# Performance work log

Hardware: AMD Instinct MI355X
Metric: run time of the kernel (lower is better)

## Reference

```python
import jax, jax.numpy as jnp
import numpy as np

N_HEAD = 12


def setup_inputs() -> dict:
    key = jax.random.key(0)
    k1, k2, k3 = jax.random.split(key, 3)
    B, T, C = 1, 4096, 768
    x = jax.random.normal(k1, (B, T, C), dtype=jnp.float32)
    w_attn = jax.random.normal(k2, (C, 3 * C), dtype=jnp.float32) * (1.0 / np.sqrt(C))
    w_proj = jax.random.normal(k3, (C, C), dtype=jnp.float32) * (1.0 / np.sqrt(C))
    return {"x": x, "w_attn": w_attn, "w_proj": w_proj}


def reference(x, w_attn, w_proj):
    B, T, C = x.shape
    hd = C // N_HEAD
    qkv = x @ w_attn  # [B, T, 3C]
    q, k, v = jnp.split(qkv, 3, axis=-1)
    # [B, H, T, hd]
    q = q.reshape(B, T, N_HEAD, hd).transpose(0, 2, 1, 3)
    k = k.reshape(B, T, N_HEAD, hd).transpose(0, 2, 1, 3)
    v = v.reshape(B, T, N_HEAD, hd).transpose(0, 2, 1, 3)
    scale = 1.0 / np.sqrt(hd).astype(np.float32)
    att = jnp.einsum('bhtd,bhsd->bhts', q, k) * scale  # materialized TxT scores
    causal = jnp.tril(jnp.ones((T, T), dtype=bool))
    att = jnp.where(causal[None, None], att, -jnp.inf)
    att = jax.nn.softmax(att, axis=-1)
    y = jnp.einsum('bhts,bhsd->bhtd', att, v)  # [B, H, T, hd]
    y = y.transpose(0, 2, 1, 3).reshape(B, T, C)
    return y @ w_proj
```

## Files before the change

kernel.cpp:

```cpp
#include <hip/hip_runtime.h>


typedef short bf16x8 __attribute__((ext_vector_type(8)));
typedef float f32x4 __attribute__((ext_vector_type(4)));

#define T_SEQ 4096
#define C_DIM 768
#define NH 12
#define HD 64

__device__ __forceinline__ unsigned short f2bf(float f) {
  union { float f; unsigned u; } v; v.f = f;
  unsigned r = v.u + 0x7FFFu + ((v.u >> 16) & 1u);
  return (unsigned short)(r >> 16);
}
__device__ __forceinline__ float bf2f(unsigned short u) {
  union { unsigned u; float f; } v; v.u = ((unsigned)u) << 16;
  return v.f;
}
__device__ __forceinline__ unsigned cvtpk(float a, float b) {
  unsigned r;
  asm("v_cvt_pk_bf16_f32 %0, %1, %2" : "=v"(r) : "v"(a), "v"(b));
  return r;
}
#define E2(x) __builtin_amdgcn_exp2f(x)

#define GLD16(g, l) __builtin_amdgcn_global_load_lds( \
    (const __attribute__((address_space(1))) void*)(g), \
    (__attribute__((address_space(3))) void*)(l), 16, 0, 0)

__device__ __forceinline__ void tr_body(const float* __restrict__ in,
                                        unsigned short* __restrict__ out,
                                        int R, int Cc, int bx, int by,
                                        float (*tile)[33]) {
  int tx = threadIdx.x & 31, ty = threadIdx.x >> 5;
#pragma unroll
  for (int i = 0; i < 32; i += 8)
    tile[ty + i][tx] = in[(size_t)(by * 32 + ty + i) * Cc + bx * 32 + tx];
  __syncthreads();
#pragma unroll
  for (int i = 0; i < 32; i += 8)
    out[(size_t)(bx * 32 + ty + i) * R + by * 32 + tx] = f2bf(tile[tx][ty + i]);
}

__global__ void prep(const float* __restrict__ x, unsigned short* __restrict__ Xb,
                     const float* __restrict__ w_attn, unsigned short* __restrict__ WaT,
                     const float* __restrict__ w_proj, unsigned short* __restrict__ WpT) {
  __shared__ float tile[32][33];
  const int bid = blockIdx.x;
  if (bid < 3072) {
    int i = (bid * 256 + threadIdx.x) * 4;
    float4 v = *reinterpret_cast<const float4*>(x + i);
    ushort4 o;
    o.x = f2bf(v.x); o.y = f2bf(v.y); o.z = f2bf(v.z); o.w = f2bf(v.w);
    *reinterpret_cast<ushort4*>(Xb + i) = o;
  } else if (bid < 3072 + 1728) {
    int b = bid - 3072;
    tr_body(w_attn, WaT, 768, 2304, b % 72, b / 72, tile);
  } else {
    int b = bid - 4800;
    tr_body(w_proj, WpT, 768, 768, b % 24, b / 24, tile);
  }
}

template <int MODE, int BM, int BN>
__global__ __launch_bounds__(256, 4)
void gemm_bt(const unsigned short* __restrict__ A,
             const unsigned short* __restrict__ Bt,
             void* __restrict__ out0,
             unsigned short* __restrict__ Kout,
             unsigned short* __restrict__ Vt,
             int M, int N, int K) {
  __shared__ __align__(16) unsigned short As[BM * 64];
  __shared__ __align__(16) unsigned short Bs[BN * 64];
  constexpr int AM = BM / 32, AN = BN / 32;
  const int nbn = N / BN;
  const int nwg = (M / BM) * nbn;
  const int cpx = nwg >> 3;
  const int swz = ((int)blockIdx.x & 7) * cpx + ((int)blockIdx.x >> 3);
  const int bm = swz / nbn, bn = swz % nbn;
  const int tid = threadIdx.x;
  const int wid = tid >> 6, lane = tid & 63;
  const int wr = wid >> 1, wc = wid & 1;
  const int lr = lane & 15;
  const int lk8 = (lane >> 4) * 8;
  const int rsub = lane >> 3, csub = (lane & 7) * 8;

  f32x4 acc[AM][AN] = {};

  const int nk = K / 64;
  for (int kt = 0; kt < nk; ++kt) {
    __syncthreads();
    {
      const unsigned short* gA = A + (size_t)(bm * BM) * K + kt * 64;
      const unsigned short* gB = Bt + (size_t)(bn * BN) * K + kt * 64;
#pragma unroll
      for (int c = 0; c < BM / 32; ++c) {
        int seg = wid * (BM / 32) + c;
        int row = seg * 8 + rsub;
        GLD16(gA + (size_t)row * K + csub, (char*)As + seg * 1024);
      }
#pragma unroll
      for (int c = 0; c < BN / 32; ++c) {
        int seg = wid * (BN / 32) + c;
        int row = seg * 8 + rsub;
        GLD16(gB + (size_t)row * K + csub, (char*)Bs + seg * 1024);
      }
    }
    __syncthreads();
#pragma unroll
    for (int kk = 0; kk < 2; ++kk) {
      bf16x8 a[AM], b[AN];
      int lk = kk * 32 + lk8;
#pragma unroll
      for (int m = 0; m < AM; ++m)
        a[m] = *reinterpret_cast<const bf16x8*>(&As[(wr * (BM / 2) + m * 16 + lr) * 64 + lk]);
#pragma unroll
      for (int n = 0; n < AN; ++n)
        b[n] = *reinterpret_cast<const bf16x8*>(&Bs[(wc * (BN / 2) + n * 16 + lr) * 64 + lk]);
#pragma unroll
      for (int m = 0; m < AM; ++m)
#pragma unroll
        for (int n = 0; n < AN; ++n)
          acc[m][n] = __builtin_amdgcn_mfma_f32_16x16x32_bf16(a[m], b[n], acc[m][n], 0, 0, 0);
    }
  }

  const int row0 = bm * BM + wr * (BM / 2);
  const int col0 = bn * BN + wc * (BN / 2);
  const int g = lane >> 4;

  if constexpr (MODE == 0) {
    if (bn * BN >= 1536) {
      __shared__ unsigned short Vst[64][72];
      const int dl0 = wc * (BN / 2);
      const int tl0 = wr * (BM / 2);
#pragma unroll
      for (int m = 0; m < AM; ++m)
#pragma unroll
        for (int n = 0; n < AN; ++n) {
          uint2 pk;
          pk.x = cvtpk(acc[m][n][0], acc[m][n][1]);
          pk.y = cvtpk(acc[m][n][2], acc[m][n][3]);
          *reinterpret_cast<uint2*>(&Vst[dl0 + n * 16 + lr][tl0 + m * 16 + g * 4]) = pk;
        }
      __syncthreads();
      const int dl = tid >> 2;
      const int tb = (tid & 3) * 16;
      uint4 a0 = *reinterpret_cast<const uint4*>(&Vst[dl][tb]);
      uint4 a1 = *reinterpret_cast<const uint4*>(&Vst[dl][tb + 8]);
      unsigned short* dst = Vt + (size_t)(bn * BN - 1536 + dl) * M + bm * BM + tb;
      *reinterpret_cast<uint4*>(dst) = a0;
      *reinterpret_cast<uint4*>(dst + 8) = a1;
      return;
    }
  }

#pragma unroll
  for (int m = 0; m < AM; ++m)
#pragma unroll
    for (int n = 0; n < AN; ++n)
#pragma unroll
      for (int j = 0; j < 4; ++j) {
        int r = row0 + m * 16 + g * 4 + j;
        int c = col0 + n * 16 + lr;
        float v = acc[m][n][j];
        if (MODE == 0) {
          if (c < 768)
            ((unsigned short*)out0)[(size_t)r * 768 + c] = f2bf(v * 0.180336884f);
          else
            Kout[(size_t)r * 768 + (c - 768)] = f2bf(v);
        } else {
          ((float*)out0)[(size_t)r * N + c] = v;
        }
      }
}

__device__ __forceinline__ void stage_k(const unsigned short* __restrict__ Kb,
                                        unsigned short* Kbuf,
                                        int h, int st, int wid, int lane) {
  const int cg = lane & 7, rsub = (lane >> 3) & 7;
  const unsigned short* gK = Kb + (size_t)(st * 64) * C_DIM + h * 64;
#pragma unroll
  for (int c = 0; c < 2; ++c) {
    int seg = wid * 2 + c;
    int row = seg * 8 + rsub;
    GLD16(gK + (size_t)row * C_DIM + (cg ^ rsub) * 8, (char*)Kbuf + seg * 1024);
  }
}
__device__ __forceinline__ void stage_v(const unsigned short* __restrict__ Vt,
                                        unsigned short* Vbuf,
                                        int h, int st, int wid, int lane) {
  const int cg = lane & 7, rsub = (lane >> 3) & 7;
  const unsigned short* gV = Vt + (size_t)(h * 64) * T_SEQ + st * 64;
#pragma unroll
  for (int c = 0; c < 2; ++c) {
    int seg = wid * 2 + c;
    int row = seg * 8 + rsub;
    GLD16(gV + (size_t)row * T_SEQ + (cg ^ rsub) * 8, (char*)Vbuf + seg * 1024);
  }
}

__device__ __forceinline__ int nchunks(int q) { return (2 * q + 13) / 12; }
__device__ __forceinline__ int part_off(int qb) {
  if (qb < 12) return (qb - 6) * 2;
  if (qb < 18) return 12 + (qb - 12) * 3;
  if (qb < 24) return 30 + (qb - 18) * 4;
  if (qb < 30) return 54 + (qb - 24) * 5;
  return 84 + (qb - 30) * 6;
}
__device__ __forceinline__ unsigned short* part_ptr(char* pA, char* pB, int set) {
  return (set < 768) ? (unsigned short*)(pA + (size_t)set * 16384)
                     : (unsigned short*)(pB + (size_t)(set - 768) * 16384);
}

__global__ __launch_bounds__(256, 3)
void attn_fwd(const unsigned short* __restrict__ Qb,
              const unsigned short* __restrict__ Kb,
              const unsigned short* __restrict__ Vt,
              unsigned short* __restrict__ Y,
              char* __restrict__ partA, char* __restrict__ partB,
              float* __restrict__ ml) {
  __shared__ __align__(16) unsigned short Ks[2][64 * 64];
  __shared__ __align__(16) unsigned short Vs[64 * 64];
  __shared__ __align__(16) unsigned short Ps[4][32 * 64];

  const int h = blockIdx.x;
  int qb = 0, ck = 0;
  {
    int idx = blockIdx.y;
    for (int q = 31; q >= 0; --q) {
      int nc = nchunks(q);
      if (idx < nc) { qb = q; ck = idx; break; }
      idx -= nc;
    }
  }
  const int nch = nchunks(qb);
  const int q0 = qb * 128;
  const int nst_total = 2 * qb + 2;
  const int st0 = ck * 12;
  const int st1 = (st0 + 12 < nst_total) ? st0 + 12 : nst_total;

  const int tid = threadIdx.x;
  const int wid = tid >> 6, lane = tid & 63;
  const int l15 = lane & 15, g = lane >> 4;
  const int sw = l15 & 7;
  const int qw = q0 + wid * 32;

  bf16x8 qf[2][2];
#pragma unroll
  for (int m = 0; m < 2; ++m)
#pragma unroll
    for (int kk = 0; kk < 2; ++kk)
      qf[m][kk] = *reinterpret_cast<const bf16x8*>(
          &Qb[(size_t)(qw + m * 16 + l15) * C_DIM + h * 64 + kk * 32 + g * 8]);

  bf16x8 ones;
#pragma unroll
  for (int e = 0; e < 8; ++e) ones[e] = (short)0x3F80;

  f32x4 o[2][4] = {};
  f32x4 po[2] = {};
  float mrow[2] = {-1e30f, -1e30f};

  stage_k(Kb, Ks[0], h, st0, wid, lane);
  stage_v(Vt, Vs, h, st0, wid, lane);
  int cur = 0;

  for (int st = st0; st < st1; ++st) {
    const bool haveNext = (st + 1 < st1);
    if (haveNext) {
      stage_k(Kb, Ks[cur ^ 1], h, st + 1, wid, lane);
      asm volatile("s_waitcnt vmcnt(2)" ::: "memory");
    } else {
      asm volatile("s_waitcnt vmcnt(0)" ::: "memory");
    }
    __builtin_amdgcn_s_barrier();

    const bool active = (st * 64) <= (qw + 31);
    if (active) {
      const unsigned short* K_ = Ks[cur];

      f32x4 sT[2][4] = {};
      __builtin_amdgcn_s_setprio(1);
#pragma unroll
      for (int kk = 0; kk < 2; ++kk) {
        bf16x8 kf[4];
#pragma unroll
        for (int n = 0; n < 4; ++n)
          kf[n] = *reinterpret_cast<const bf16x8*>(
              &K_[(n * 16 + l15) * 64 + (((kk * 4 + g) ^ sw) * 8)]);
#pragma unroll
        for (int m = 0; m < 2; ++m)
#pragma unroll
          for (int n = 0; n < 4; ++n)
            sT[m][n] = __builtin_amdgcn_mfma_f32_16x16x32_bf16(kf[n], qf[m][kk], sT[m][n], 0, 0, 0);
      }
      __builtin_amdgcn_s_setprio(0);

      unsigned short* Pw = Ps[wid];
#pragma unroll
      for (int m = 0; m < 2; ++m) {
        if (!(st * 64 + 63 <= qw + m * 16)) {
          const int bound = (qw + m * 16 + l15) - st * 64;
#pragma unroll
          for (int n = 0; n < 4; ++n)
#pragma unroll
            for (int jj = 0; jj < 4; ++jj) {
              int sl = n * 16 + g * 4 + jj;
              if (sl > bound) sT[m][n][jj] = -1e30f;
            }
        }
        float vm[4];
#pragma unroll
        for (int n = 0; n < 4; ++n)
          vm[n] = fmaxf(fmaxf(sT[m][n][0], sT[m][n][1]), fmaxf(sT[m][n][2], sT[m][n][3]));
        float vmax = fmaxf(fmaxf(vm[0], vm[1]), fmaxf(vm[2], vm[3]));
        vmax = fmaxf(vmax, __shfl_xor(vmax, 16, 64));
        vmax = fmaxf(vmax, __shfl_xor(vmax, 32, 64));
        const bool defer = (__all(vmax <= mrow[m] + 8.0f) != 0);
        const float mnew = defer ? mrow[m] : fmaxf(mrow[m], vmax);
#pragma unroll
        for (int n = 0; n < 4; ++n)
#pragma unroll
          for (int jj = 0; jj < 4; ++jj)
            sT[m][n][jj] = E2(sT[m][n][jj] - mnew);
        if (!defer) {
          float alpha = E2(mrow[m] - mnew);
          mrow[m] = mnew;
#pragma unroll
          for (int n2 = 0; n2 < 4; ++n2) o[m][n2] *= alpha;
          po[m] *= alpha;
        }
#pragma unroll
        for (int n = 0; n < 4; ++n) {
          uint2 pw;
          pw.x = cvtpk(sT[m][n][0], sT[m][n][1]);
          pw.y = cvtpk(sT[m][n][2], sT[m][n][3]);
          *reinterpret_cast<uint2*>(
              &Pw[(m * 16 + l15) * 64 + (((n * 2 + (g >> 1)) ^ sw) * 8) + (g & 1) * 4]) = pw;
        }
      }
      asm volatile("s_waitcnt lgkmcnt(0)" ::: "memory");

      __builtin_amdgcn_s_setprio(1);
#pragma unroll
      for (int ks = 0; ks < 2; ++ks) {
        bf16x8 vf[4], pf[2];
#pragma unroll
        for (int n2 = 0; n2 < 4; ++n2)
          vf[n2] = *reinterpret_cast<const bf16x8*>(
              &Vs[(n2 * 16 + l15) * 64 + (((ks * 4 + g) ^ sw) * 8)]);
#pragma unroll
        for (int m = 0; m < 2; ++m)
          pf[m] = *reinterpret_cast<const bf16x8*>(
              &Pw[(m * 16 + l15) * 64 + (((ks * 4 + g) ^ sw) * 8)]);
#pragma unroll
        for (int m = 0; m < 2; ++m) {
#pragma unroll
          for (int n2 = 0; n2 < 4; ++n2)
            o[m][n2] = __builtin_amdgcn_mfma_f32_16x16x32_bf16(vf[n2], pf[m], o[m][n2], 0, 0, 0);
          po[m] = __builtin_amdgcn_mfma_f32_16x16x32_bf16(ones, pf[m], po[m], 0, 0, 0);
        }
      }
      __builtin_amdgcn_s_setprio(0);
    }
    asm volatile("" ::: "memory");
    __builtin_amdgcn_s_barrier();
    if (haveNext) stage_v(Vt, Vs, h, st + 1, wid, lane);
    cur ^= 1;
  }

  if (nch == 1) {
#pragma unroll
    for (int m = 0; m < 2; ++m) {
      float inv = 1.0f / po[m][0];
      int qg = qw + m * 16 + l15;
#pragma unroll
      for (int n2 = 0; n2 < 4; ++n2) {
        uint2 yk;
        yk.x = cvtpk(o[m][n2][0] * inv, o[m][n2][1] * inv);
        yk.y = cvtpk(o[m][n2][2] * inv, o[m][n2][3] * inv);
        *reinterpret_cast<uint2*>(&Y[(size_t)qg * C_DIM + h * 64 + n2 * 16 + g * 4]) = yk;
      }
    }
  } else {
    const int set = h * 96 + part_off(qb) + ck;
    unsigned short* po_ = part_ptr(partA, partB, set);
#pragma unroll
    for (int m = 0; m < 2; ++m) {
      int qL = wid * 32 + m * 16 + l15;
#pragma unroll
      for (int n2 = 0; n2 < 4; ++n2) {
        uint2 pk;
        pk.x = cvtpk(o[m][n2][0], o[m][n2][1]);
        pk.y = cvtpk(o[m][n2][2], o[m][n2][3]);
        *reinterpret_cast<uint2*>(&po_[qL * 64 + n2 * 16 + g * 4]) = pk;
      }
      if (g == 0) {
        ml[(size_t)set * 256 + qL * 2] = mrow[m];
        ml[(size_t)set * 256 + qL * 2 + 1] = po[m][0];
      }
    }
  }
}

__global__ __launch_bounds__(256)
void attn_combine(char* __restrict__ partA, char* __restrict__ partB,
                  const float* __restrict__ ml, unsigned short* __restrict__ Y) {
  const int qb = 6 + blockIdx.x;
  const int h = blockIdx.y;
  const int nch = nchunks(qb);
  const int set0 = h * 96 + part_off(qb);
  const int t = threadIdx.x;
  const int r = t >> 1, dh = (t & 1) * 32;

  float mi[6], li[6];
  float M = -1e30f;
  for (int i = 0; i < nch; ++i) {
    mi[i] = ml[(size_t)(set0 + i) * 256 + r * 2];
    li[i] = ml[(size_t)(set0 + i) * 256 + r * 2 + 1];
    M = fmaxf(M, mi[i]);
  }
  float L = 0.f;
  float O[32];
#pragma unroll
  for (int d = 0; d < 32; ++d) O[d] = 0.f;
  for (int i = 0; i < nch; ++i) {
    float w = E2(mi[i] - M);
    L += li[i] * w;
    const unsigned short* po = part_ptr(partA, partB, set0 + i) + r * 64 + dh;
#pragma unroll
    for (int d4 = 0; d4 < 32; d4 += 4) {
      ushort4 v = *reinterpret_cast<const ushort4*>(po + d4);
      O[d4 + 0] += bf2f(v.x) * w;
      O[d4 + 1] += bf2f(v.y) * w;
      O[d4 + 2] += bf2f(v.z) * w;
      O[d4 + 3] += bf2f(v.w) * w;
    }
  }
  float inv = 1.0f / L;
  unsigned short* yp = Y + (size_t)(qb * 128 + r) * C_DIM + h * 64 + dh;
#pragma unroll
  for (int d4 = 0; d4 < 32; d4 += 4) {
    uint2 yk;
    yk.x = cvtpk(O[d4 + 0] * inv, O[d4 + 1] * inv);
    yk.y = cvtpk(O[d4 + 2] * inv, O[d4 + 3] * inv);
    *reinterpret_cast<uint2*>(yp + d4) = yk;
  }
}

extern "C" void kernel_launch(void* const* d_in, const int* in_sizes, int n_in,
                              void* d_out, int out_size, void* d_ws, size_t ws_size,
                              hipStream_t stream) {
  const float* x = (const float*)d_in[0];
  const float* w_attn = (const float*)d_in[1];
  const float* w_proj = (const float*)d_in[2];
  float* out = (float*)d_out;

  char* ws = (char*)d_ws;
  unsigned short* Xb   = (unsigned short*)(ws + 0);
  unsigned short* WaT  = (unsigned short*)(ws + 6291456);
  unsigned short* WpT  = (unsigned short*)(ws + 9830400);
  unsigned short* Qb   = (unsigned short*)(ws + 11010048);
  unsigned short* Kb   = (unsigned short*)(ws + 17301504);
  unsigned short* Vt   = (unsigned short*)(ws + 23592960);
  unsigned short* Yb   = (unsigned short*)(ws + 29884416);

  char* partA = (char*)d_out;
  char* partB = (char*)ws;
  float* mlp  = (float*)(ws + 6291456);

  prep<<<5376, 256, 0, stream>>>(x, Xb, w_attn, WaT, w_proj, WpT);

  gemm_bt<0, 64, 64><<<(T_SEQ / 64) * (2304 / 64), 256, 0, stream>>>(
      Xb, WaT, (void*)Qb, Kb, Vt, T_SEQ, 2304, C_DIM);

  attn_fwd<<<dim3(NH, 102), 256, 0, stream>>>(Qb, Kb, Vt, Yb, partA, partB, mlp);
  attn_combine<<<dim3(26, NH), 256, 0, stream>>>(partA, partB, mlp, Yb);

  gemm_bt<1, 64, 64><<<(T_SEQ / 64) * (C_DIM / 64), 256, 0, stream>>>(
      Yb, WpT, (void*)out, nullptr, nullptr, T_SEQ, C_DIM, C_DIM);
}
```

Baseline: 126.1 us.

## Double-buffer GEMM shared-memory tiles to overlap global loads with MFMA

Converts the bf16 GEMM main loop from single-buffered to double-buffered LDS staging. The next K-tile is prefetched with direct-to-LDS loads while the current tile is consumed, using a partial vmcnt wait and raw barriers instead of two full __syncthreads. The V-transpose staging buffer now aliases the shared tile memory. This doubles LDS per workgroup, which may reduce occupancy at the requested launch bounds.

```diff
diff --git a/kernel.cpp b/kernel.cpp
--- a/kernel.cpp
+++ b/kernel.cpp
@@ -71,8 +71,7 @@
              unsigned short* __restrict__ Kout,
              unsigned short* __restrict__ Vt,
              int M, int N, int K) {
-  __shared__ __align__(16) unsigned short As[BM * 64];
-  __shared__ __align__(16) unsigned short Bs[BN * 64];
+  __shared__ __align__(16) unsigned short smem[2 * (BM + BN) * 64];
   constexpr int AM = BM / 32, AN = BN / 32;
   const int nbn = N / BN;
   const int nwg = (M / BM) * nbn;
@@ -86,28 +85,48 @@
   const int lk8 = (lane >> 4) * 8;
   const int rsub = lane >> 3, csub = (lane & 7) * 8;
 
+  auto Abuf = [&](int b) { return smem + b * BM * 64; };
+  auto Bbuf = [&](int b) { return smem + 2 * BM * 64 + b * BN * 64; };
+
   f32x4 acc[AM][AN] = {};
-
   const int nk = K / 64;
+
+  auto STAGE = [&](int kt, int buf) {
+    const unsigned short* gA = A + (size_t)(bm * BM) * K + kt * 64;
+    const unsigned short* gB = Bt + (size_t)(bn * BN) * K + kt * 64;
+#pragma unroll
+    for (int c = 0; c < BM / 32; ++c) {
+      int seg = wid * (BM / 32) + c;
+      int row = seg * 8 + rsub;
+      GLD16(gA + (size_t)row * K + csub, (char*)Abuf(buf) + seg * 1024);
+    }
+#pragma unroll
+    for (int c = 0; c < BN / 32; ++c) {
+      int seg = wid * (BN / 32) + c;
+      int row = seg * 8 + rsub;
+      GLD16(gB + (size_t)row * K + csub, (char*)Bbuf(buf) + seg * 1024);
+    }
+  };
+
+  STAGE(0, 0);
+  int cur = 0;
   for (int kt = 0; kt < nk; ++kt) {
-    __syncthreads();
-    {
-      const unsigned short* gA = A + (size_t)(bm * BM) * K + kt * 64;
-      const unsigned short* gB = Bt + (size_t)(bn * BN) * K + kt * 64;
-#pragma unroll
-      for (int c = 0; c < BM / 32; ++c) {
-        int seg = wid * (BM / 32) + c;
-        int row = seg * 8 + rsub;
-        GLD16(gA + (size_t)row * K + csub, (char*)As + seg * 1024);
-      }
-#pragma unroll
-      for (int c = 0; c < BN / 32; ++c) {
-        int seg = wid * (BN / 32) + c;
-        int row = seg * 8 + rsub;
-        GLD16(gB + (size_t)row * K + csub, (char*)Bs + seg * 1024);
-      }
-    }
-    __syncthreads();
+    if (kt + 1 < nk) {
+      STAGE(kt + 1, cur ^ 1);
+      constexpr int LOADS = BM / 32 + BN / 32;
+      if constexpr (LOADS == 4)
+        asm volatile("s_waitcnt vmcnt(4)" ::: "memory");
+      else if constexpr (LOADS == 6)
+        asm volatile("s_waitcnt vmcnt(6)" ::: "memory");
+      else
+        asm volatile("s_waitcnt vmcnt(0)" ::: "memory");
+    } else {
+      asm volatile("s_waitcnt vmcnt(0)" ::: "memory");
+    }
+    __builtin_amdgcn_s_barrier();
+
+    const unsigned short* As = Abuf(cur);
+    const unsigned short* Bs = Bbuf(cur);
 #pragma unroll
     for (int kk = 0; kk < 2; ++kk) {
       bf16x8 a[AM], b[AN];
@@ -124,6 +143,9 @@
         for (int n = 0; n < AN; ++n)
           acc[m][n] = __builtin_amdgcn_mfma_f32_16x16x32_bf16(a[m], b[n], acc[m][n], 0, 0, 0);
     }
+    asm volatile("" ::: "memory");
+    __builtin_amdgcn_s_barrier();
+    cur ^= 1;
   }
 
   const int row0 = bm * BM + wr * (BM / 2);
@@ -132,7 +154,8 @@
 
   if constexpr (MODE == 0) {
     if (bn * BN >= 1536) {
-      __shared__ unsigned short Vst[64][72];
+      __syncthreads();
+      unsigned short (*Vst)[72] = reinterpret_cast<unsigned short (*)[72]>(smem);
       const int dl0 = wc * (BN / 2);
       const int tl0 = wr * (BM / 2);
 #pragma unroll
```

After: 120.1 us, median of 2. 1.05x faster.
